# Performance work log

Hardware: AMD Instinct MI355X
Metric: run time of the kernel (lower is better)

Reference implementation:

```python
import jax, jax.numpy as jnp
import numpy as np

# Config (matches init_kwargs)
B, L, D = 2, 2048, 1024
QH, KVH, HD, FFN = 8, 2, 128, 4096
EPS = 1.1920929e-07  # torch RMSNorm default eps = finfo(float32).eps


def _rope_ts():
    d2 = HD // 2
    freq_exp = (2.0 / HD) * jnp.arange(d2, dtype=jnp.float32)
    return 10000.0 ** freq_exp  # [d2]


def _rope(x):
    # x: [B, L, H, HD], rotated in fp32 (matches x.float() in source)
    d2 = HD // 2
    pos = jnp.arange(L, dtype=jnp.float32)
    rad = pos[:, None] / _rope_ts()[None, :]          # [L, d2]
    s = jnp.sin(rad)[None, :, None, :]                # [1, L, 1, d2]
    c = jnp.cos(rad)[None, :, None, :]
    xf = x.astype(jnp.float32)
    x1, x2 = xf[..., :d2], xf[..., d2:]
    return jnp.concatenate([x1 * c - x2 * s, x2 * c + x1 * s], axis=-1).astype(x.dtype)


def _rmsnorm(x, w):
    xf = x.astype(jnp.float32)
    r = jax.lax.rsqrt(jnp.mean(xf * xf, axis=-1, keepdims=True) + EPS)
    return (xf * r).astype(x.dtype) * w


def setup_inputs() -> dict:
    key = jax.random.key(0)
    ks = jax.random.split(key, 9)
    s = 0.02
    return {
        "x": jax.random.normal(ks[0], (B, L, D), dtype=jnp.float32),
        "ln1_w": jnp.ones((D,), dtype=jnp.float32),
        "wq": jax.random.normal(ks[1], (D, QH * HD), dtype=jnp.float32) * s,
        "wk": jax.random.normal(ks[2], (D, KVH * HD), dtype=jnp.float32) * s,
        "wv": jax.random.normal(ks[3], (D, KVH * HD), dtype=jnp.float32) * s,
        "wo": jax.random.normal(ks[4], (QH * HD, D), dtype=jnp.float32) * s,
        "ln2_w": jnp.ones((D,), dtype=jnp.float32),
        "wg": jax.random.normal(ks[5], (D, FFN), dtype=jnp.float32) * s,
        "wu": jax.random.normal(ks[6], (D, FFN), dtype=jnp.float32) * s,
        "wd": jax.random.normal(ks[7], (FFN, D), dtype=jnp.float32) * s,
    }


def reference(x, ln1_w, wq, wk, wv, wo, ln2_w, wg, wu, wd):
    residual = x
    h = _rmsnorm(x, ln1_w)

    q = _rope((h @ wq).reshape(B, L, QH, HD))          # [B,L,QH,HD]
    k = _rope((h @ wk).reshape(B, L, KVH, HD))         # [B,L,KVH,HD]
    v = (h @ wv).reshape(B, L, KVH, HD)

    rep = QH // KVH  # kv_map = floor(arange(QH)*KVH/QH) == repeat each kv head `rep` times
    qh = jnp.transpose(q, (0, 2, 1, 3)).astype(jnp.float32)                       # [B,QH,L,HD]
    kh = jnp.transpose(jnp.repeat(k, rep, axis=2), (0, 2, 1, 3)).astype(jnp.float32)
    vh = jnp.transpose(jnp.repeat(v, rep, axis=2), (0, 2, 1, 3)).astype(jnp.float32)

    scores = jnp.einsum("bhqd,bhkd->bhqk", qh, kh) / jnp.sqrt(jnp.float32(HD))    # [B,QH,L,L]
    causal = jnp.triu(jnp.ones((L, L), dtype=bool), 1)
    scores = jnp.where(causal, -jnp.inf, scores)
    attn = jax.nn.softmax(scores, axis=-1)
    ctx = jnp.einsum("bhqk,bhkd->bhqd", attn, vh)                                 # [B,QH,L,HD]
    ctx = jnp.transpose(ctx, (0, 2, 1, 3)).reshape(B, L, QH * HD).astype(x.dtype)

    x = ctx @ wo + residual
    residual = x
    h = _rmsnorm(x, ln2_w)
    return (jax.nn.silu(h @ wg) * (h @ wu)) @ wd + residual
```

## Files before the change

kernel.cpp:

```cpp
#include <hip/hip_runtime.h>
#include <hip/hip_bf16.h>
#include <math.h>

#define B_ 2
#define L_ 2048
#define D_ 1024
#define QH_ 8
#define KVH_ 2
#define HD_ 128
#define FFN_ 4096
#define T_ (B_ * L_)
#define EPS_ 1.1920929e-07f

typedef __bf16 bf16x8 __attribute__((ext_vector_type(8)));
typedef float floatx4 __attribute__((ext_vector_type(4)));
typedef unsigned short ushortx8 __attribute__((ext_vector_type(8)));
typedef unsigned short ushortx4 __attribute__((ext_vector_type(4)));

__device__ __forceinline__ unsigned short f2bf(float f) {
  union { float f; unsigned int u; } v;
  v.f = f;
  unsigned int r = v.u + 0x7FFFu + ((v.u >> 16) & 1u);
  return (unsigned short)(r >> 16);
}
__device__ __forceinline__ float bf2f(unsigned short u) {
  union { unsigned int u; float f; } v;
  v.u = ((unsigned int)u) << 16;
  return v.f;
}
__device__ __forceinline__ void gload_lds16(const void* g, void* l) {
  __builtin_amdgcn_global_load_lds((const __attribute__((address_space(1))) void*)g,
                                   (__attribute__((address_space(3))) void*)l, 16, 0, 0);
}

__device__ __forceinline__ void strip_tc(const float* __restrict__ in,
                                         unsigned short* __restrict__ out,
                                         int K, int N, int n0, int k0) {
  __shared__ float tile[4][32][33];
  int t = threadIdx.x;
  int tx = t & 31, ty = t >> 5;
#pragma unroll
  for (int s = 0; s < 4; s++)
#pragma unroll
    for (int r0 = 0; r0 < 4; r0++) {
      int r = ty + r0 * 8;
      tile[s][r][tx] = in[(size_t)(k0 + s * 32 + r) * N + n0 + tx];
    }
  __syncthreads();
  int nr = t >> 3, kq = t & 7;
#pragma unroll
  for (int s = 0; s < 4; s++) {
    ushortx4 o4;
#pragma unroll
    for (int j = 0; j < 4; j++) o4[j] = f2bf(tile[s][kq * 4 + j][nr]);
    *(ushortx4*)(out + (size_t)(n0 + nr) * K + k0 + s * 32 + kq * 4) = o4;
  }
}

__device__ __forceinline__ void rmsnorm_row(const float* __restrict__ x,
                                            const float* __restrict__ w,
                                            unsigned short* __restrict__ o, int row) {
  __shared__ float red[4];
  int t = threadIdx.x;
  const float* xr = x + (size_t)row * D_;
  float4 xv = *(const float4*)(xr + t * 4);
  float ss = xv.x * xv.x + xv.y * xv.y + xv.z * xv.z + xv.w * xv.w;
#pragma unroll
  for (int off = 32; off >= 1; off >>= 1) ss += __shfl_xor(ss, off);
  if ((t & 63) == 0) red[t >> 6] = ss;
  __syncthreads();
  float total = red[0] + red[1] + red[2] + red[3];
  float r = rsqrtf(total * (1.0f / (float)D_) + EPS_);
  float4 wv = *(const float4*)(w + t * 4);
  unsigned short* op = o + (size_t)row * D_ + t * 4;
  op[0] = f2bf(xv.x * r * wv.x);
  op[1] = f2bf(xv.y * r * wv.y);
  op[2] = f2bf(xv.z * r * wv.z);
  op[3] = f2bf(xv.w * r * wv.w);
}

__global__ __launch_bounds__(256) void prep_all(
    const float* __restrict__ wq, const float* __restrict__ wk,
    const float* __restrict__ wv, const float* __restrict__ wo,
    const float* __restrict__ wg, const float* __restrict__ wu,
    const float* __restrict__ wd, unsigned short* __restrict__ wT,
    const float* __restrict__ x, const float* __restrict__ ln1w,
    unsigned short* __restrict__ h_bf) {
  int bid = blockIdx.x;
  if (bid < 3712) {
    const float* in;
    unsigned short* out;
    int K, N, nt, base;
    if (bid < 256)       { in = wq; out = wT;            K = 1024; N = 1024; nt = 32;  base = 0; }
    else if (bid < 320)  { in = wk; out = wT + 1048576;  K = 1024; N = 256;  nt = 8;   base = 256; }
    else if (bid < 384)  { in = wv; out = wT + 1310720;  K = 1024; N = 256;  nt = 8;   base = 320; }
    else if (bid < 640)  { in = wo; out = wT + 1572864;  K = 1024; N = 1024; nt = 32;  base = 384; }
    else if (bid < 1664) { in = wg; out = wT + 2621440;  K = 1024; N = 4096; nt = 128; base = 640; }
    else if (bid < 2688) { in = wu; out = wT + 6815744;  K = 1024; N = 4096; nt = 128; base = 1664; }
    else                 { in = wd; out = wT + 11010048; K = 4096; N = 1024; nt = 32;  base = 2688; }
    int idx = bid - base;
    strip_tc(in, out, K, N, (idx % nt) * 32, (idx / nt) * 128);
  } else {
    rmsnorm_row(x, ln1w, h_bf, bid - 3712);
  }
}

__global__ __launch_bounds__(256) void rmsnorm_bf16_kernel(const float* __restrict__ x,
                                                           const float* __restrict__ w,
                                                           unsigned short* __restrict__ o) {
  rmsnorm_row(x, w, o, blockIdx.x);
}

template <int EPI, int KH>
__global__ __launch_bounds__(256, 3) void gemm_bf16(const unsigned short* __restrict__ A,
                                                    const unsigned short* __restrict__ BT,
                                                    const float* __restrict__ R,
                                                    float* __restrict__ C,
                                                    int M, int N, int K) {
  __shared__ unsigned short As[KH][64 * 32];
  __shared__ unsigned short Bs[KH][128 * 32];
  int t = threadIdx.x;
  int lane = t & 63, wave = t >> 6;
  int m0 = blockIdx.y * 64, n0 = blockIdx.x * 128;

  int row_a = t >> 2;
  int kc = ((t & 3) ^ ((t >> 3) & 3)) * 8;
  const unsigned short* ga0 = A + (size_t)(m0 + row_a) * K + kc;
  const unsigned short* gb0 = BT + (size_t)(n0 + row_a) * K + kc;
  const unsigned short* gb1 = BT + (size_t)(n0 + 64 + row_a) * K + kc;

  int wm = (wave & 1) * 32, wn = (wave >> 1) * 64;
  int fr = lane & 15, quad = lane >> 4;
  int sw = (quad ^ ((fr >> 1) & 3)) * 8;

  floatx4 acc[2][4];
#pragma unroll
  for (int i = 0; i < 2; i++)
#pragma unroll
    for (int j = 0; j < 4; j++) acc[i][j] = (floatx4){0.f, 0.f, 0.f, 0.f};

  for (int k0 = 0; k0 < K; k0 += 32 * KH) {
#pragma unroll
    for (int h = 0; h < KH; h++) {
      int ko = k0 + h * 32;
      gload_lds16(ga0 + ko, As[h] + wave * 512);
      gload_lds16(gb0 + ko, Bs[h] + wave * 512);
      gload_lds16(gb1 + ko, Bs[h] + 2048 + wave * 512);
    }
    __syncthreads();
#pragma unroll
    for (int h = 0; h < KH; h++) {
      const unsigned short* arp = As[h] + (size_t)(wm + fr) * 32 + sw;
      const unsigned short* brp = Bs[h] + (size_t)(wn + fr) * 32 + sw;
      bf16x8 af[2], bfr[4];
#pragma unroll
      for (int i = 0; i < 2; i++)
        af[i] = __builtin_bit_cast(bf16x8, *(const ushortx8*)(arp + i * 16 * 32));
#pragma unroll
      for (int j = 0; j < 4; j++)
        bfr[j] = __builtin_bit_cast(bf16x8, *(const ushortx8*)(brp + j * 16 * 32));
#pragma unroll
      for (int i = 0; i < 2; i++)
#pragma unroll
        for (int j = 0; j < 4; j++)
          acc[i][j] = __builtin_amdgcn_mfma_f32_16x16x32_bf16(af[i], bfr[j], acc[i][j], 0, 0, 0);
    }
    __syncthreads();
  }

  int orow = m0 + wm + quad * 4;
  int ocol = n0 + wn + fr;
#pragma unroll
  for (int i = 0; i < 2; i++) {
#pragma unroll
    for (int r = 0; r < 4; r++) {
      int row = orow + i * 16 + r;
#pragma unroll
      for (int j = 0; j < 4; j++) {
        size_t idx = (size_t)row * N + ocol + j * 16;
        float v = acc[i][j][r];
        if (EPI == 1) C[idx] = v + R[idx];
        else C[idx] = v + C[idx];
      }
    }
  }
}

__global__ __launch_bounds__(256) void gemm_qkv(const unsigned short* __restrict__ A,
                                                const unsigned short* __restrict__ BT,
                                                unsigned short* __restrict__ qb,
                                                unsigned short* __restrict__ Kb,
                                                unsigned short* __restrict__ Vt) {
  constexpr int K = 1024;
  __shared__ unsigned short smem[24576];
  int t = threadIdx.x;
  int lane = t & 63, wave = t >> 6;
  int bx = blockIdx.x;
  int m0 = blockIdx.y * 64, n0 = bx * 128;

  int row_a = t >> 2;
  int kc = ((t & 3) ^ ((t >> 3) & 3)) * 8;
  const unsigned short* ga0 = A + (size_t)(m0 + row_a) * K + kc;
  const unsigned short* gb0 = BT + (size_t)(n0 + row_a) * K + kc;
  const unsigned short* gb1 = BT + (size_t)(n0 + 64 + row_a) * K + kc;

  int wm = (wave & 1) * 32, wn = (wave >> 1) * 64;
  int fr = lane & 15, quad = lane >> 4;
  int sw = (quad ^ ((fr >> 1) & 3)) * 8;

  floatx4 acc[2][4];
#pragma unroll
  for (int i = 0; i < 2; i++)
#pragma unroll
    for (int j = 0; j < 4; j++) acc[i][j] = (floatx4){0.f, 0.f, 0.f, 0.f};

  for (int k0 = 0; k0 < K; k0 += 128) {
#pragma unroll
    for (int h = 0; h < 4; h++) {
      int ko = k0 + h * 32;
      gload_lds16(ga0 + ko, smem + h * 2048 + wave * 512);
      gload_lds16(gb0 + ko, smem + 8192 + h * 4096 + wave * 512);
      gload_lds16(gb1 + ko, smem + 8192 + h * 4096 + 2048 + wave * 512);
    }
    __syncthreads();
#pragma unroll
    for (int h = 0; h < 4; h++) {
      const unsigned short* arp = smem + h * 2048 + (size_t)(wm + fr) * 32 + sw;
      const unsigned short* brp = smem + 8192 + h * 4096 + (size_t)(wn + fr) * 32 + sw;
      bf16x8 af[2], bfr[4];
#pragma unroll
      for (int i = 0; i < 2; i++)
        af[i] = __builtin_bit_cast(bf16x8, *(const ushortx8*)(arp + i * 16 * 32));
#pragma unroll
      for (int j = 0; j < 4; j++)
        bfr[j] = __builtin_bit_cast(bf16x8, *(const ushortx8*)(brp + j * 16 * 32));
#pragma unroll
      for (int i = 0; i < 2; i++)
#pragma unroll
        for (int j = 0; j < 4; j++)
          acc[i][j] = __builtin_amdgcn_mfma_f32_16x16x32_bf16(af[i], bfr[j], acc[i][j], 0, 0, 0);
    }
    __syncthreads();
  }

  unsigned short* scr = smem;
#pragma unroll
  for (int i = 0; i < 2; i++)
#pragma unroll
    for (int r = 0; r < 4; r++)
#pragma unroll
      for (int j = 0; j < 4; j++)
        scr[(size_t)(wm + quad * 4 + i * 16 + r) * 136 + wn + fr + j * 16] =
            f2bf(acc[i][j][r]);
  __syncthreads();

  if (bx < 10) {
    int row = t >> 2, dq = (t & 3) * 16;
    int tok = m0 + row, pos = tok & (L_ - 1), b = tok >> 11;
    float scale_ = (bx < 8) ? 0.08838834764831843f : 1.0f;
    unsigned short lo[16], hi[16];
#pragma unroll
    for (int m = 0; m < 16; m++) {
      int d2 = dq + m;
      float x1 = bf2f(scr[(size_t)row * 136 + d2]);
      float x2 = bf2f(scr[(size_t)row * 136 + d2 + 64]);
      float inv_ts = expf(-0.14391156831f * (float)d2);
      float rad = (float)pos * inv_ts;
      float s = sinf(rad), c = cosf(rad);
      lo[m] = f2bf((x1 * c - x2 * s) * scale_);
      hi[m] = f2bf((x2 * c + x1 * s) * scale_);
    }
    if (bx < 8) {
      unsigned short* dst = qb + (size_t)tok * 1024 + bx * 128;
      *(ushortx8*)(dst + dq) = *(const ushortx8*)(lo);
      *(ushortx8*)(dst + dq + 8) = *(const ushortx8*)(lo + 8);
      *(ushortx8*)(dst + 64 + dq) = *(const ushortx8*)(hi);
      *(ushortx8*)(dst + 64 + dq + 8) = *(const ushortx8*)(hi + 8);
    } else {
      int kvh = bx - 8, bk = b * KVH_ + kvh, swk = pos & 15;
      unsigned short* dst = Kb + ((size_t)bk * L_ + pos) * HD_;
      int c0 = dq >> 3;
      *(ushortx8*)(dst + ((c0) ^ swk) * 8) = *(const ushortx8*)(lo);
      *(ushortx8*)(dst + ((c0 + 1) ^ swk) * 8) = *(const ushortx8*)(lo + 8);
      *(ushortx8*)(dst + ((c0 + 8) ^ swk) * 8) = *(const ushortx8*)(hi);
      *(ushortx8*)(dst + ((c0 + 9) ^ swk) * 8) = *(const ushortx8*)(hi + 8);
    }
  } else {
    int kvh = bx - 10;
    int b = m0 >> 11, key0 = m0 & (L_ - 1), bk = b * KVH_ + kvh;
    int hd = t >> 1, half = t & 1;
#pragma unroll
    for (int c = 0; c < 4; c++) {
      int cp = half * 4 + c, kcc = cp ^ (hd & 7);
      ushortx8 ob;
#pragma unroll
      for (int j = 0; j < 8; j++) ob[j] = scr[(size_t)(kcc * 8 + j) * 136 + hd];
      *(ushortx8*)(Vt + ((size_t)bk * HD_ + hd) * L_ + key0 + cp * 8) = ob;
    }
  }
}

__global__ __launch_bounds__(512, 2) void gemm_gateup8(
    const unsigned short* __restrict__ A,
    const unsigned short* __restrict__ BgT,
    const unsigned short* __restrict__ BuT,
    unsigned short* __restrict__ Cb) {
  constexpr int K = 1024;
  constexpr int NTILES = K / 32;
  __shared__ unsigned short As[4][256 * 32];
  __shared__ unsigned short Bs[4][256 * 32];

  int t = threadIdx.x;
  int lane = t & 63, wave = t >> 6;
  int m0 = blockIdx.y * 256;
  int n0l = blockIdx.x * 128;

  int row_a = t >> 2;
  int kc = ((t & 3) ^ ((t >> 3) & 3)) * 8;
  const unsigned short* ga0 = A + (size_t)(m0 + row_a) * K + kc;
  const unsigned short* ga1 = ga0 + (size_t)128 * K;
  int rb0 = row_a, rb1 = row_a + 128;
  const unsigned short* gb0 =
      ((rb0 & 31) < 16 ? BgT : BuT) +
      (size_t)(n0l + (rb0 >> 5) * 16 + (rb0 & 15)) * K + kc;
  const unsigned short* gb1 =
      ((rb1 & 31) < 16 ? BgT : BuT) +
      (size_t)(n0l + (rb1 >> 5) * 16 + (rb1 & 15)) * K + kc;

  int wm = wave >> 2;
  int wn = wave & 3;
  int fr = lane & 15, quad = lane >> 4;
  int sw = (quad ^ ((fr >> 1) & 3)) * 8;

  floatx4 acc[8][4];
#pragma unroll
  for (int i = 0; i < 8; i++)
#pragma unroll
    for (int j = 0; j < 4; j++) acc[i][j] = (floatx4){0.f, 0.f, 0.f, 0.f};

#define GU_STAGE(kt_)                                              \
  {                                                                \
    int ko_ = (kt_) * 32;                                          \
    unsigned short* as_ = (unsigned short*)As[(kt_) & 3];          \
    unsigned short* bs_ = (unsigned short*)Bs[(kt_) & 3];          \
    gload_lds16(ga0 + ko_, as_ + wave * 512);                      \
    gload_lds16(ga1 + ko_, as_ + 4096 + wave * 512);               \
    gload_lds16(gb0 + ko_, bs_ + wave * 512);                      \
    gload_lds16(gb1 + ko_, bs_ + 4096 + wave * 512);               \
  }

#define GU_COMPUTE(kt_)                                                        \
  {                                                                            \
    const unsigned short* asr = As[(kt_) & 3];                                 \
    const unsigned short* bsr = Bs[(kt_) & 3];                                 \
    bf16x8 bfr[4], af[8];                                                      \
    _Pragma("unroll") for (int j = 0; j < 4; j++) bfr[j] =                     \
        __builtin_bit_cast(bf16x8,                                             \
            *(const ushortx8*)(bsr + (size_t)(wn * 64 + j * 16 + fr) * 32 + sw)); \
    _Pragma("unroll") for (int i = 0; i < 8; i++) af[i] =                      \
        __builtin_bit_cast(bf16x8,                                             \
            *(const ushortx8*)(asr + (size_t)(wm * 128 + i * 16 + fr) * 32 + sw)); \
    __builtin_amdgcn_s_setprio(1);                                             \
    _Pragma("unroll") for (int i = 0; i < 8; i++)                              \
        _Pragma("unroll") for (int j = 0; j < 4; j++) acc[i][j] =              \
            __builtin_amdgcn_mfma_f32_16x16x32_bf16(af[i], bfr[j], acc[i][j],  \
                                                    0, 0, 0);                  \
    __builtin_amdgcn_s_setprio(0);                                             \
  }

  GU_STAGE(0);
  GU_STAGE(1);
  GU_STAGE(2);

  for (int kt = 0; kt < NTILES - 2; kt++) {
    asm volatile("s_waitcnt vmcnt(8)" ::: "memory");
    __builtin_amdgcn_s_barrier();
    asm volatile("" ::: "memory");
    if (kt < NTILES - 3) GU_STAGE(kt + 3);
    GU_COMPUTE(kt);
  }
  asm volatile("s_waitcnt vmcnt(4)" ::: "memory");
  __builtin_amdgcn_s_barrier();
  asm volatile("" ::: "memory");
  GU_COMPUTE(NTILES - 2);
  asm volatile("s_waitcnt vmcnt(0)" ::: "memory");
  __builtin_amdgcn_s_barrier();
  asm volatile("" ::: "memory");
  GU_COMPUTE(NTILES - 1);

#undef GU_STAGE
#undef GU_COMPUTE

#pragma unroll
  for (int i = 0; i < 8; i++) {
    int row = m0 + wm * 128 + i * 16 + quad * 4;
#pragma unroll
    for (int r = 0; r < 4; r++) {
#pragma unroll
      for (int jj = 0; jj < 2; jj++) {
        float g = acc[i][2 * jj][r];
        float u = acc[i][2 * jj + 1][r];
        int colL = n0l + (wn * 2 + jj) * 16 + fr;
        Cb[(size_t)(row + r) * FFN_ + colL] = f2bf(g / (1.f + __expf(-g)) * u);
      }
    }
  }
}

__global__ __launch_bounds__(256) void attn_mfma(const unsigned short* __restrict__ qb,
                                                 const unsigned short* __restrict__ Kb,
                                                 const unsigned short* __restrict__ Vt,
                                                 unsigned short* __restrict__ ctx) {
  __shared__ unsigned short Ks[64 * 128];
  __shared__ unsigned short Vs[128 * 64];
  __shared__ unsigned short Ps[4][16 * 72];
  int id = blockIdx.x;
  int bh = id & 15;
  int p_ = id >> 4;
  int qt = (p_ < 16) ? p_ : 47 - p_;
  int b = bh >> 3, h = bh & 7;
  int bk = b * KVH_ + (h >> 2);
  int q0 = qt * 64;
  int t = threadIdx.x, lane = t & 63, w = t >> 6;
  int fr = lane & 15, quad = lane >> 4;

  int pos = q0 + w * 16 + fr;
  const unsigned short* qrow = qb + (size_t)(b * L_ + pos) * 1024 + h * HD_;
  bf16x8 qf[4];
#pragma unroll
  for (int kb = 0; kb < 4; kb++)
    qf[kb] = __builtin_bit_cast(bf16x8, *(const ushortx8*)(qrow + kb * 32 + quad * 8));

  floatx4 o_acc[8];
#pragma unroll
  for (int nt = 0; nt < 8; nt++) o_acc[nt] = (floatx4){0.f, 0.f, 0.f, 0.f};
  float l_r[4] = {0.f, 0.f, 0.f, 0.f};
  unsigned short* Psw = Ps[w];
  const unsigned short* kgb = Kb + (size_t)bk * L_ * HD_;
  const unsigned short* vgb = Vt + (size_t)bk * HD_ * L_;
  int rowg0 = q0 + w * 16 + quad * 4;

  for (int kt = 0; kt <= qt; kt++) {
    int kstart = kt * 64;
    bool diag = (kt == qt);
    __syncthreads();
    const unsigned short* ksrc = kgb + (size_t)kstart * HD_;
#pragma unroll
    for (int it = 0; it < 4; it++) {
      int sl = it * 4 + w;
      gload_lds16(ksrc + sl * 512 + lane * 8, Ks + sl * 512);
    }
#pragma unroll
    for (int it = 0; it < 4; it++) {
      int sl = it * 4 + w;
      gload_lds16(vgb + (size_t)(sl * 8 + (lane >> 3)) * L_ + kstart + (lane & 7) * 8,
                  Vs + sl * 512);
    }
    __syncthreads();

    floatx4 s_acc[4];
#pragma unroll
    for (int jt = 0; jt < 4; jt++) s_acc[jt] = (floatx4){0.f, 0.f, 0.f, 0.f};
#pragma unroll
    for (int kb = 0; kb < 4; kb++) {
#pragma unroll
      for (int jt = 0; jt < 4; jt++) {
        bf16x8 kf = __builtin_bit_cast(
            bf16x8, *(const ushortx8*)(Ks + (jt * 16 + fr) * 128 +
                                       (((kb * 4 + quad) ^ fr) * 8)));
        s_acc[jt] = __builtin_amdgcn_mfma_f32_16x16x32_bf16(qf[kb], kf, s_acc[jt], 0, 0, 0);
      }
    }

#pragma unroll
    for (int jt = 0; jt < 4; jt++) {
#pragma unroll
      for (int r = 0; r < 4; r++) {
        float pp;
        if (diag) {
          int keyg = kstart + jt * 16 + fr;
          pp = (keyg <= rowg0 + r) ? __expf(s_acc[jt][r]) : 0.f;
        } else {
          pp = __expf(s_acc[jt][r]);
        }
        l_r[r] += pp;
        Psw[(quad * 4 + r) * 72 + jt * 16 + fr] = f2bf(pp);
      }
    }
    bf16x8 pf0 = __builtin_bit_cast(bf16x8, *(const ushortx8*)(Psw + fr * 72 + quad * 8));
    bf16x8 pf1 =
        __builtin_bit_cast(bf16x8, *(const ushortx8*)(Psw + fr * 72 + 32 + quad * 8));
#pragma unroll
    for (int nt = 0; nt < 8; nt++) {
      bf16x8 vf0 = __builtin_bit_cast(
          bf16x8,
          *(const ushortx8*)(Vs + (nt * 16 + fr) * 64 + ((quad ^ (fr & 7)) * 8)));
      bf16x8 vf1 = __builtin_bit_cast(
          bf16x8,
          *(const ushortx8*)(Vs + (nt * 16 + fr) * 64 + (((4 + quad) ^ (fr & 7)) * 8)));
      o_acc[nt] = __builtin_amdgcn_mfma_f32_16x16x32_bf16(pf0, vf0, o_acc[nt], 0, 0, 0);
      o_acc[nt] = __builtin_amdgcn_mfma_f32_16x16x32_bf16(pf1, vf1, o_acc[nt], 0, 0, 0);
    }
  }

#pragma unroll
  for (int r = 0; r < 4; r++) {
    l_r[r] += __shfl_xor(l_r[r], 1);
    l_r[r] += __shfl_xor(l_r[r], 2);
    l_r[r] += __shfl_xor(l_r[r], 4);
    l_r[r] += __shfl_xor(l_r[r], 8);
  }

  unsigned short* ob =
      ctx + (size_t)(b * L_ + q0 + w * 16 + quad * 4) * 1024 + h * HD_ + fr;
#pragma unroll
  for (int r = 0; r < 4; r++) {
    float inv = 1.f / l_r[r];
    unsigned short* orow = ob + (size_t)r * 1024;
#pragma unroll
    for (int nt = 0; nt < 8; nt++) orow[nt * 16] = f2bf(o_acc[nt][r] * inv);
  }
}

extern "C" void kernel_launch(void* const* d_in, const int* in_sizes, int n_in,
                              void* d_out, int out_size, void* d_ws, size_t ws_size,
                              hipStream_t stream) {
  const float* x    = (const float*)d_in[0];
  const float* ln1w = (const float*)d_in[1];
  const float* wq   = (const float*)d_in[2];
  const float* wk   = (const float*)d_in[3];
  const float* wvp  = (const float*)d_in[4];
  const float* wo   = (const float*)d_in[5];
  const float* ln2w = (const float*)d_in[6];
  const float* wg   = (const float*)d_in[7];
  const float* wu   = (const float*)d_in[8];
  const float* wd   = (const float*)d_in[9];
  float* out = (float*)d_out;
  char* ws = (char*)d_ws;

  unsigned short* wT = (unsigned short*)ws;
  unsigned short* wqkvT = wT;
  unsigned short* woT = wT + 1572864;
  unsigned short* wgT = wT + 2621440;
  unsigned short* wuT = wT + 6815744;
  unsigned short* wdT = wT + 11010048;
  unsigned short* h_bf = (unsigned short*)(ws + 30408704);
  unsigned short* qb = (unsigned short*)(ws + 38797312);
  unsigned short* h2_bf = (unsigned short*)(ws + 51380224);
  unsigned short* Kb = (unsigned short*)(ws + 59768832);
  unsigned short* Vt = (unsigned short*)(ws + 61865984);
  unsigned short* gu = (unsigned short*)(ws + 59768832);
  unsigned short* ctx_bf = h_bf;

  dim3 blk(256);

  prep_all<<<3712 + T_, blk, 0, stream>>>(wq, wk, wvp, wo, wg, wu, wd, wT, x, ln1w, h_bf);
  gemm_qkv<<<dim3(12, 64), blk, 0, stream>>>(h_bf, wqkvT, qb, Kb, Vt);
  attn_mfma<<<512, blk, 0, stream>>>(qb, Kb, Vt, ctx_bf);
  gemm_bf16<1, 4><<<dim3(8, 64), blk, 0, stream>>>(ctx_bf, woT, x, out, T_, 1024, 1024);
  rmsnorm_bf16_kernel<<<T_, blk, 0, stream>>>(out, ln2w, h2_bf);
  gemm_gateup8<<<dim3(32, 16), dim3(512), 0, stream>>>(h2_bf, wgT, wuT, gu);
  gemm_bf16<2, 4><<<dim3(8, 64), blk, 0, stream>>>(gu, wdT, nullptr, out, T_, 1024, FFN_);
}
```

Baseline: 380.1 us.

## Shrink gate/up GEMM tile to 128x256 with 256 threads and triple buffering

Replaces the 512-thread gate/up GEMM, which used a 256x256 tile and a 4-stage LDS pipeline, with a 256-thread kernel using a 128-row by 256-column tile and a 3-stage pipeline. Each wave now covers all 128 rows against its own 64 columns. The grid doubles to 1024 blocks, giving better CU coverage and lower LDS use per block. The cost is less operand reuse per block, more redundant B-tile loads from global memory, and one fewer stage of prefetch depth.

New measurement: 368.5 us. 1.03x faster.

```diff
diff --git a/kernel.cpp b/kernel.cpp
--- a/kernel.cpp
+++ b/kernel.cpp
@@ -300,37 +300,36 @@
   }
 }
 
-__global__ __launch_bounds__(512, 2) void gemm_gateup8(
+__global__ __launch_bounds__(256, 2) void gemm_gateup3(
     const unsigned short* __restrict__ A,
     const unsigned short* __restrict__ BgT,
     const unsigned short* __restrict__ BuT,
     unsigned short* __restrict__ Cb) {
   constexpr int K = 1024;
-  constexpr int NTILES = K / 32;
-  __shared__ unsigned short As[4][256 * 32];
-  __shared__ unsigned short Bs[4][256 * 32];
+  constexpr int NT = 32;
+  __shared__ unsigned short As[3][128 * 32];
+  __shared__ unsigned short Bs[3][256 * 32];
 
   int t = threadIdx.x;
   int lane = t & 63, wave = t >> 6;
-  int m0 = blockIdx.y * 256;
+  int m0 = blockIdx.y * 128;
   int n0l = blockIdx.x * 128;
 
   int row_a = t >> 2;
   int kc = ((t & 3) ^ ((t >> 3) & 3)) * 8;
   const unsigned short* ga0 = A + (size_t)(m0 + row_a) * K + kc;
-  const unsigned short* ga1 = ga0 + (size_t)128 * K;
-  int rb0 = row_a, rb1 = row_a + 128;
-  const unsigned short* gb0 =
-      ((rb0 & 31) < 16 ? BgT : BuT) +
-      (size_t)(n0l + (rb0 >> 5) * 16 + (rb0 & 15)) * K + kc;
-  const unsigned short* gb1 =
-      ((rb1 & 31) < 16 ? BgT : BuT) +
-      (size_t)(n0l + (rb1 >> 5) * 16 + (rb1 & 15)) * K + kc;
-
-  int wm = wave >> 2;
-  int wn = wave & 3;
+  const unsigned short* ga1 = ga0 + (size_t)64 * K;
+  const unsigned short* gb[4];
+#pragma unroll
+  for (int q = 0; q < 4; q++) {
+    int rb = q * 64 + row_a;
+    const unsigned short* src = ((rb & 31) < 16) ? BgT : BuT;
+    gb[q] = src + (size_t)(n0l + (rb >> 5) * 16 + (rb & 15)) * K + kc;
+  }
+
   int fr = lane & 15, quad = lane >> 4;
   int sw = (quad ^ ((fr >> 1) & 3)) * 8;
+  int wn = wave;
 
   floatx4 acc[8][4];
 #pragma unroll
@@ -338,62 +337,56 @@
 #pragma unroll
     for (int j = 0; j < 4; j++) acc[i][j] = (floatx4){0.f, 0.f, 0.f, 0.f};
 
-#define GU_STAGE(kt_)                                              \
-  {                                                                \
-    int ko_ = (kt_) * 32;                                          \
-    unsigned short* as_ = (unsigned short*)As[(kt_) & 3];          \
-    unsigned short* bs_ = (unsigned short*)Bs[(kt_) & 3];          \
-    gload_lds16(ga0 + ko_, as_ + wave * 512);                      \
-    gload_lds16(ga1 + ko_, as_ + 4096 + wave * 512);               \
-    gload_lds16(gb0 + ko_, bs_ + wave * 512);                      \
-    gload_lds16(gb1 + ko_, bs_ + 4096 + wave * 512);               \
-  }
-
-#define GU_COMPUTE(kt_)                                                        \
-  {                                                                            \
-    const unsigned short* asr = As[(kt_) & 3];                                 \
-    const unsigned short* bsr = Bs[(kt_) & 3];                                 \
-    bf16x8 bfr[4], af[8];                                                      \
-    _Pragma("unroll") for (int j = 0; j < 4; j++) bfr[j] =                     \
-        __builtin_bit_cast(bf16x8,                                             \
-            *(const ushortx8*)(bsr + (size_t)(wn * 64 + j * 16 + fr) * 32 + sw)); \
-    _Pragma("unroll") for (int i = 0; i < 8; i++) af[i] =                      \
-        __builtin_bit_cast(bf16x8,                                             \
-            *(const ushortx8*)(asr + (size_t)(wm * 128 + i * 16 + fr) * 32 + sw)); \
-    __builtin_amdgcn_s_setprio(1);                                             \
-    _Pragma("unroll") for (int i = 0; i < 8; i++)                              \
-        _Pragma("unroll") for (int j = 0; j < 4; j++) acc[i][j] =              \
-            __builtin_amdgcn_mfma_f32_16x16x32_bf16(af[i], bfr[j], acc[i][j],  \
-                                                    0, 0, 0);                  \
-    __builtin_amdgcn_s_setprio(0);                                             \
+#define GU_STAGE(kt_)                                       \
+  {                                                         \
+    int ko_ = (kt_) * 32;                                   \
+    int bi_ = (kt_) % 3;                                    \
+    gload_lds16(ga0 + ko_, As[bi_] + wave * 512);           \
+    gload_lds16(ga1 + ko_, As[bi_] + 2048 + wave * 512);    \
+    gload_lds16(gb[0] + ko_, Bs[bi_] + wave * 512);         \
+    gload_lds16(gb[1] + ko_, Bs[bi_] + 2048 + wave * 512);  \
+    gload_lds16(gb[2] + ko_, Bs[bi_] + 4096 + wave * 512);  \
+    gload_lds16(gb[3] + ko_, Bs[bi_] + 6144 + wave * 512);  \
+  }
+
+#define GU_COMPUTE(kt_)                                                          \
+  {                                                                              \
+    const unsigned short* asr = As[(kt_) % 3];                                   \
+    const unsigned short* bsr = Bs[(kt_) % 3] + wn * 64 * 32;                    \
+    bf16x8 af[8], bfr[4];                                                        \
+    _Pragma("unroll") for (int j = 0; j < 4; j++) bfr[j] = __builtin_bit_cast(   \
+        bf16x8, *(const ushortx8*)(bsr + (size_t)(j * 16 + fr) * 32 + sw));      \
+    _Pragma("unroll") for (int i = 0; i < 8; i++) af[i] = __builtin_bit_cast(    \
+        bf16x8, *(const ushortx8*)(asr + (size_t)(i * 16 + fr) * 32 + sw));      \
+    __builtin_amdgcn_s_setprio(1);                                               \
+    _Pragma("unroll") for (int i = 0; i < 8; i++)                                \
+        _Pragma("unroll") for (int j = 0; j < 4; j++) acc[i][j] =                \
+            __builtin_amdgcn_mfma_f32_16x16x32_bf16(af[i], bfr[j], acc[i][j],    \
+                                                    0, 0, 0);                    \
+    __builtin_amdgcn_s_setprio(0);                                               \
   }
 
   GU_STAGE(0);
   GU_STAGE(1);
-  GU_STAGE(2);
-
-  for (int kt = 0; kt < NTILES - 2; kt++) {
-    asm volatile("s_waitcnt vmcnt(8)" ::: "memory");
+
+  for (int kt = 0; kt < NT - 1; kt++) {
+    asm volatile("s_waitcnt vmcnt(6)" ::: "memory");
     __builtin_amdgcn_s_barrier();
     asm volatile("" ::: "memory");
-    if (kt < NTILES - 3) GU_STAGE(kt + 3);
+    if (kt < NT - 2) GU_STAGE(kt + 2);
     GU_COMPUTE(kt);
   }
-  asm volatile("s_waitcnt vmcnt(4)" ::: "memory");
-  __builtin_amdgcn_s_barrier();
-  asm volatile("" ::: "memory");
-  GU_COMPUTE(NTILES - 2);
   asm volatile("s_waitcnt vmcnt(0)" ::: "memory");
   __builtin_amdgcn_s_barrier();
   asm volatile("" ::: "memory");
-  GU_COMPUTE(NTILES - 1);
+  GU_COMPUTE(NT - 1);
 
 #undef GU_STAGE
 #undef GU_COMPUTE
 
 #pragma unroll
   for (int i = 0; i < 8; i++) {
-    int row = m0 + wm * 128 + i * 16 + quad * 4;
+    int row = m0 + i * 16 + quad * 4;
 #pragma unroll
     for (int r = 0; r < 4; r++) {
 #pragma unroll
@@ -559,6 +552,6 @@
   attn_mfma<<<512, blk, 0, stream>>>(qb, Kb, Vt, ctx_bf);
   gemm_bf16<1, 4><<<dim3(8, 64), blk, 0, stream>>>(ctx_bf, woT, x, out, T_, 1024, 1024);
   rmsnorm_bf16_kernel<<<T_, blk, 0, stream>>>(out, ln2w, h2_bf);
-  gemm_gateup8<<<dim3(32, 16), dim3(512), 0, stream>>>(h2_bf, wgT, wuT, gu);
+  gemm_gateup3<<<dim3(32, 32), blk, 0, stream>>>(h2_bf, wgT, wuT, gu);
   gemm_bf16<2, 4><<<dim3(8, 64), blk, 0, stream>>>(gu, wdT, nullptr, out, T_, 1024, FFN_);
 }
```
